# Kernel tuning notes

Hardware: AMD Instinct MI355X
Metric: run time of the kernel (lower is better)

## Reference

```python
import jax, jax.numpy as jnp
import numpy as np

DIM = 768
HEADS = 12
B, H_IMG, W_IMG = 8, 32, 32


def setup_inputs() -> dict:
    key = jax.random.key(0)
    k1, k2, k3 = jax.random.split(key, 3)
    x = jax.random.normal(k1, (B, DIM, H_IMG, W_IMG), dtype=jnp.float32)
    w_qkv = jax.random.normal(k2, (DIM, 3 * DIM), dtype=jnp.float32) * (DIM ** -0.5)
    w_proj = jax.random.normal(k3, (DIM, DIM), dtype=jnp.float32) * (DIM ** -0.5)
    return {"x": x, "w_qkv": w_qkv, "w_proj": w_proj}


def reference(x, w_qkv, w_proj):
    b, c, h, w = x.shape
    n = h * w
    d_head = c // HEADS
    # NOTE: original multiplies energy by sqrt(d_head) (not divides) -- kept faithful.
    scale = d_head ** 0.5

    tokens = x.reshape(b, c, n).transpose(0, 2, 1)          # (b, n, c)
    qkv = tokens @ w_qkv                                     # (b, n, 3c)
    # einops '(d k h)': d outermost, k middle, h innermost
    qkv = qkv.reshape(b, n, d_head, 3, HEADS)
    qkv = jnp.transpose(qkv, (3, 0, 4, 1, 2))                # (3, b, heads, n, d)
    q, k, v = qkv[0], qkv[1], qkv[2]

    energy = jnp.einsum('bhid,bhjd->bhij', q, k) * scale     # (b, heads, n, n)
    attn = jax.nn.softmax(energy, axis=-1)
    ctx = jnp.einsum('bhij,bhjd->bhid', attn, v)             # (b, heads, n, d)
    ctx = jnp.transpose(ctx, (0, 2, 1, 3)).reshape(b, n, c)  # (b, n, c) = (h d) concat
    out = ctx @ w_proj                                       # (b, n, c)
    return jnp.transpose(out.reshape(b, h, w, c), (0, 3, 1, 2))  # (b, c, h, w)
```

## Files before the change

### kernel.cpp

```cpp
#include <hip/hip_runtime.h>

#define NB    8
#define CDIM  768
#define NTOK  1024
#define NHEAD 12
#define DHEAD 64
#define C3    2304

typedef unsigned short u16;
typedef short  s8v __attribute__((ext_vector_type(8)));
typedef float  f4v __attribute__((ext_vector_type(4)));

#define MFMA16(a, b, c) __builtin_amdgcn_mfma_f32_16x16x32_bf16((a), (b), (c), 0, 0, 0)

static __device__ __forceinline__ u16 f2bf(float f) {
    unsigned u = __float_as_uint(f);
    u += 0x7fffu + ((u >> 16) & 1u);
    return (u16)(u >> 16);
}
static __device__ __forceinline__ float bf2f(u16 b) {
    return __uint_as_float(((unsigned)b) << 16);
}
static __device__ __forceinline__ unsigned packsplit(float x) {
    u16 h = f2bf(x);
    u16 l = f2bf(x - bf2f(h));
    return (unsigned)h | ((unsigned)l << 16);
}
static __device__ __forceinline__ void unpack8(uint4 a, uint4 b, s8v& h, s8v& l) {
    h = (s8v){(short)a.x, (short)a.y, (short)a.z, (short)a.w,
              (short)b.x, (short)b.y, (short)b.z, (short)b.w};
    l = (s8v){(short)(a.x >> 16), (short)(a.y >> 16), (short)(a.z >> 16), (short)(a.w >> 16),
              (short)(b.x >> 16), (short)(b.y >> 16), (short)(b.z >> 16), (short)(b.w >> 16)};
}
static __device__ __forceinline__ int sw32i(int row, int k) {
    int g = (k >> 3) & 3;
    int gs = g ^ ((row >> 1) & 3);
    return (k & ~31) + (gs << 3) + (k & 7);
}
static __device__ __forceinline__ void gload16(const u16* gsrc, u16* ldst) {
    __builtin_amdgcn_global_load_lds(
        (const __attribute__((address_space(1))) void*)gsrc,
        (__attribute__((address_space(3))) void*)ldst, 16, 0, 0);
}

__launch_bounds__(256)
__global__ void split_x(const float* __restrict__ x,
                        u16* __restrict__ xh, u16* __restrict__ xl) {
    __shared__ float Tf[64][65];
    const int t  = threadIdx.x;
    const int p0 = blockIdx.x * 64;
    const int c0 = blockIdx.y * 64;
    const int b  = blockIdx.z;

    #pragma unroll
    for (int i = 0; i < 4; ++i) {
        int cl = (t >> 4) + i * 16;
        int pl = (t & 15) * 4;
        float4 v4 = *(const float4*)&x[((size_t)(b * CDIM) + c0 + cl) * NTOK + p0 + pl];
        Tf[cl][pl + 0] = v4.x; Tf[cl][pl + 1] = v4.y;
        Tf[cl][pl + 2] = v4.z; Tf[cl][pl + 3] = v4.w;
    }
    __syncthreads();
    #pragma unroll
    for (int i = 0; i < 4; ++i) {
        int pr = (t >> 4) + i * 16;
        int c4 = (t & 15) * 4;
        u16 hs[4], ls[4];
        #pragma unroll
        for (int j = 0; j < 4; ++j) {
            float val = Tf[c4 + j][pr];
            hs[j] = f2bf(val);
            ls[j] = f2bf(val - bf2f(hs[j]));
        }
        size_t m = (size_t)(b * NTOK) + p0 + pr;
        int ksw = sw32i(p0 + pr, c0 + c4);
        *(ushort4*)&xh[m * CDIM + ksw] = make_ushort4(hs[0], hs[1], hs[2], hs[3]);
        *(ushort4*)&xl[m * CDIM + ksw] = make_ushort4(ls[0], ls[1], ls[2], ls[3]);
    }
}

__launch_bounds__(256)
__global__ void split_w(const float* __restrict__ w,
                        u16* __restrict__ wh, u16* __restrict__ wl) {
    __shared__ float Wf[16][148];
    const int t  = threadIdx.x;
    const int d0 = blockIdx.x * 4;
    const int c0 = blockIdx.y * 16;

    #pragma unroll
    for (int i = 0; i < 9; ++i) {
        int idx = t + i * 256;
        int cl = idx / 144;
        int nl = idx - cl * 144;
        Wf[cl][nl] = w[(size_t)(c0 + cl) * C3 + d0 * 36 + nl];
    }
    __syncthreads();
    #pragma unroll
    for (int i = 0; i < 9; ++i) {
        int idx = t + i * 256;
        int r  = idx >> 4;
        int cc = idx & 15;
        int dd = r / 36;
        int th = r - dd * 36;
        float val = Wf[cc][dd * 36 + th];
        u16 hb = f2bf(val);
        int np = th * 64 + d0 + dd;
        size_t o = (size_t)np * CDIM + sw32i(np, c0 + cc);
        wh[o] = hb;
        wl[o] = f2bf(val - bf2f(hb));
    }
}

__launch_bounds__(256)
__global__ void split_wp(const float* __restrict__ w,
                         u16* __restrict__ wph, u16* __restrict__ wpl) {
    __shared__ float Tf[64][65];
    const int t  = threadIdx.x;
    const int n0 = blockIdx.x * 64;
    const int k0 = blockIdx.y * 64;

    #pragma unroll
    for (int i = 0; i < 4; ++i) {
        int kl = (t >> 4) + i * 16;
        int nl = (t & 15) * 4;
        float4 v4 = *(const float4*)&w[(size_t)(k0 + kl) * CDIM + n0 + nl];
        Tf[kl][nl + 0] = v4.x; Tf[kl][nl + 1] = v4.y;
        Tf[kl][nl + 2] = v4.z; Tf[kl][nl + 3] = v4.w;
    }
    __syncthreads();
    #pragma unroll
    for (int i = 0; i < 4; ++i) {
        int nr = (t >> 4) + i * 16;
        int k4 = (t & 15) * 4;
        u16 hs[4], ls[4];
        #pragma unroll
        for (int j = 0; j < 4; ++j) {
            float val = Tf[k4 + j][nr];
            hs[j] = f2bf(val);
            ls[j] = f2bf(val - bf2f(hs[j]));
        }
        int n = n0 + nr;
        int ksw = sw32i(n, k0 + k4);
        *(ushort4*)&wph[(size_t)n * CDIM + ksw] = make_ushort4(hs[0], hs[1], hs[2], hs[3]);
        *(ushort4*)&wpl[(size_t)n * CDIM + ksw] = make_ushort4(ls[0], ls[1], ls[2], ls[3]);
    }
}

__launch_bounds__(256)
__global__ void qkv_mfma(const u16* __restrict__ xh, const u16* __restrict__ xl,
                         const u16* __restrict__ wh, const u16* __restrict__ wl,
                         unsigned* __restrict__ Qp,
                         u16* __restrict__ Khg, u16* __restrict__ Klg,
                         u16* __restrict__ Vhg, u16* __restrict__ Vlg) {
    __shared__ u16 Ah[128][32];
    __shared__ u16 Al[128][32];
    __shared__ u16 Bh[128][32];
    __shared__ u16 Bl[128][32];

    const int tid = threadIdx.x;
    const int l   = tid & 63;
    const int w   = tid >> 6;
    const int lm  = l & 15;
    const int lg  = l >> 4;
    const int wr  = w >> 1;
    const int wc  = w & 1;
    const int m0  = blockIdx.x * 128;
    const int n0  = blockIdx.y * 128;
    const int b   = m0 >> 10;
    const int p0  = m0 & 1023;

    const size_t xbase = ((size_t)(b * NTOK) + p0) * CDIM;
    const int lrow = l >> 2;
    const int kq   = (l & 3) * 8;
    const int asw  = (lg ^ ((lm >> 1) & 3)) * 8;

    f4v acc[4][4];
    #pragma unroll
    for (int i = 0; i < 4; ++i)
        #pragma unroll
        for (int j = 0; j < 4; ++j)
            acc[i][j] = (f4v){0.f, 0.f, 0.f, 0.f};

    for (int k0 = 0; k0 < CDIM; k0 += 32) {
        #pragma unroll
        for (int i = 0; i < 2; ++i) {
            int ch = w * 2 + i;
            int m  = ch * 16 + lrow;
            int lo = ch * 512;
            gload16(xh + xbase + (size_t)m * CDIM + k0 + kq, &Ah[0][0] + lo);
            gload16(xl + xbase + (size_t)m * CDIM + k0 + kq, &Al[0][0] + lo);
            gload16(wh + (size_t)(n0 + m) * CDIM + k0 + kq,  &Bh[0][0] + lo);
            gload16(wl + (size_t)(n0 + m) * CDIM + k0 + kq,  &Bl[0][0] + lo);
        }
        __syncthreads();

        s8v ah[4], al[4], bh[4], bl[4];
        #pragma unroll
        for (int mi = 0; mi < 4; ++mi) {
            int row = wr * 64 + mi * 16 + lm;
            ah[mi] = *(const s8v*)&Ah[row][asw];
            al[mi] = *(const s8v*)&Al[row][asw];
        }
        #pragma unroll
        for (int ni = 0; ni < 4; ++ni) {
            int row = wc * 64 + ni * 16 + lm;
            bh[ni] = *(const s8v*)&Bh[row][asw];
            bl[ni] = *(const s8v*)&Bl[row][asw];
        }
        #pragma unroll
        for (int mi = 0; mi < 4; ++mi)
            #pragma unroll
            for (int ni = 0; ni < 4; ++ni) {
                acc[mi][ni] = MFMA16(ah[mi], bh[ni], acc[mi][ni]);
                acc[mi][ni] = MFMA16(ah[mi], bl[ni], acc[mi][ni]);
                acc[mi][ni] = MFMA16(al[mi], bh[ni], acc[mi][ni]);
            }
        __syncthreads();
    }

    const int th = (n0 >> 6) + wc;
    const int t3 = th / 12;
    const int h  = th - t3 * 12;
    const size_t bhb = (size_t)(b * NHEAD + h) * NTOK;

    if (t3 == 0) {
        unsigned* dst = Qp + bhb * DHEAD;
        #pragma unroll
        for (int mi = 0; mi < 4; ++mi)
            #pragma unroll
            for (int r = 0; r < 4; ++r) {
                int p = p0 + wr * 64 + mi * 16 + lg * 4 + r;
                #pragma unroll
                for (int ni = 0; ni < 4; ++ni)
                    dst[(size_t)p * DHEAD + ni * 16 + lm] = packsplit(acc[mi][ni][r] * 8.0f);
            }
    } else if (t3 == 1) {
        u16* dh = Khg + bhb * DHEAD;
        u16* dl = Klg + bhb * DHEAD;
        #pragma unroll
        for (int mi = 0; mi < 4; ++mi)
            #pragma unroll
            for (int r = 0; r < 4; ++r) {
                int p = p0 + wr * 64 + mi * 16 + lg * 4 + r;
                #pragma unroll
                for (int ni = 0; ni < 4; ++ni) {
                    int d = ni * 16 + lm;
                    int dsw = (((d >> 3) ^ (p & 7)) << 3) | (d & 7);
                    float val = acc[mi][ni][r];
                    u16 hb = f2bf(val);
                    dh[(size_t)p * DHEAD + dsw] = hb;
                    dl[(size_t)p * DHEAD + dsw] = f2bf(val - bf2f(hb));
                }
            }
    } else {
        u16* dh = Vhg + bhb * DHEAD;
        u16* dl = Vlg + bhb * DHEAD;
        #pragma unroll
        for (int mi = 0; mi < 4; ++mi)
            #pragma unroll
            for (int r = 0; r < 4; ++r) {
                int p = p0 + wr * 64 + mi * 16 + lg * 4 + r;
                #pragma unroll
                for (int ni = 0; ni < 4; ++ni) {
                    int d = ni * 16 + lm;
                    float val = acc[mi][ni][r];
                    u16 hb = f2bf(val);
                    dh[(size_t)p * DHEAD + d] = hb;
                    dl[(size_t)p * DHEAD + d] = f2bf(val - bf2f(hb));
                }
            }
    }
}

__launch_bounds__(256)
__global__ void vt_split(const u16* __restrict__ Vh, const u16* __restrict__ Vl,
                         u16* __restrict__ Vth, u16* __restrict__ Vtl) {
    __shared__ u16 Th[64][72];
    __shared__ u16 Tl[64][72];
    const int t  = threadIdx.x;
    const int pt = blockIdx.x;
    const int bh = blockIdx.y;

    #pragma unroll
    for (int i = 0; i < 4; ++i) {
        int idx = t + i * 256;
        int pr  = idx >> 4;
        int c4  = (idx & 15) * 4;
        size_t src = ((size_t)bh * NTOK + pt * 64 + pr) * DHEAD + c4;
        *(ushort4*)&Th[pr][c4] = *(const ushort4*)&Vh[src];
        *(ushort4*)&Tl[pr][c4] = *(const ushort4*)&Vl[src];
    }
    __syncthreads();
    #pragma unroll
    for (int i = 0; i < 4; ++i) {
        int idx   = t + i * 256;
        int plane = idx >> 9;
        int rem   = idx & 511;
        int d     = rem >> 3;
        int gp    = rem & 7;
        int gs    = gp ^ (d & 7);
        u16 tmp[8];
        #pragma unroll
        for (int j = 0; j < 8; ++j)
            tmp[j] = plane ? Tl[gs * 8 + j][d] : Th[gs * 8 + j][d];
        u16* outp = plane ? Vtl : Vth;
        size_t dst = ((size_t)bh * DHEAD + d) * NTOK + pt * 64 + gp * 8;
        *(ushort4*)&outp[dst]     = make_ushort4(tmp[0], tmp[1], tmp[2], tmp[3]);
        *(ushort4*)&outp[dst + 4] = make_ushort4(tmp[4], tmp[5], tmp[6], tmp[7]);
    }
}

__launch_bounds__(256)
__global__ void attn_mfma(const unsigned* __restrict__ Qp,
                          const u16* __restrict__ Khg, const u16* __restrict__ Klg,
                          const u16* __restrict__ Vth, const u16* __restrict__ Vtl,
                          u16* __restrict__ ctxh, u16* __restrict__ ctxl) {
    __shared__ u16 Kh[64][64];
    __shared__ u16 Kl[64][64];
    __shared__ u16 Vh[64][64];
    __shared__ u16 Vl[64][64];
    __shared__ u16 Ph[128][64];

    const int tid = threadIdx.x;
    const int l  = tid & 63;
    const int w  = tid >> 6;
    const int lm = l & 15;
    const int lg = l >> 4;
    const int bh = blockIdx.y;
    const int p0 = blockIdx.x * 128;

    const unsigned* Qb = Qp + (size_t)bh * NTOK * DHEAD;
    const u16* Kb_h = Khg + (size_t)bh * NTOK * DHEAD;
    const u16* Kb_l = Klg + (size_t)bh * NTOK * DHEAD;
    const u16* Vb_h = Vth + (size_t)bh * DHEAD * NTOK;
    const u16* Vb_l = Vtl + (size_t)bh * DHEAD * NTOK;

    s8v qh[2][2], ql[2][2];
    #pragma unroll
    for (int t = 0; t < 2; ++t)
        #pragma unroll
        for (int kk = 0; kk < 2; ++kk) {
            const unsigned* src = Qb + (size_t)(p0 + w * 32 + t * 16 + lm) * DHEAD + kk * 32 + lg * 8;
            uint4 a0 = *(const uint4*)src;
            uint4 a1 = *(const uint4*)(src + 4);
            unpack8(a0, a1, qh[t][kk], ql[t][kk]);
        }

    f4v o[2][4];
    float mrun[2][4], lrun[2][4];
    #pragma unroll
    for (int t = 0; t < 2; ++t)
        #pragma unroll
        for (int c = 0; c < 4; ++c)
            o[t][c] = (f4v){0.f, 0.f, 0.f, 0.f};
    #pragma unroll
    for (int t = 0; t < 2; ++t)
        #pragma unroll
        for (int i = 0; i < 4; ++i) { mrun[t][i] = -3.0e38f; lrun[t][i] = 0.f; }

    const int fsw = (l & 7) * 8;
    const int r8  = l >> 3;

    for (int kt = 0; kt < 16; ++kt) {
        __syncthreads();
        #pragma unroll
        for (int i = 0; i < 2; ++i) {
            int ch = w * 2 + i;
            int lo = ch * 512;
            size_t krow = (size_t)(kt * 64 + ch * 8 + r8) * DHEAD + fsw;
            gload16(Kb_h + krow, &Kh[0][0] + lo);
            gload16(Kb_l + krow, &Kl[0][0] + lo);
            size_t vrow = (size_t)(ch * 8 + r8) * NTOK + kt * 64 + fsw;
            gload16(Vb_h + vrow, &Vh[0][0] + lo);
            gload16(Vb_l + vrow, &Vl[0][0] + lo);
        }
        __syncthreads();

        f4v sa[2][4];
        #pragma unroll
        for (int t = 0; t < 2; ++t)
            #pragma unroll
            for (int c = 0; c < 4; ++c)
                sa[t][c] = (f4v){0.f, 0.f, 0.f, 0.f};

        #pragma unroll
        for (int kk = 0; kk < 2; ++kk)
            #pragma unroll
            for (int c = 0; c < 4; ++c) {
                int row = c * 16 + lm;
                int off = (((kk * 4 + lg) ^ (lm & 7))) * 8;
                s8v kh = *(const s8v*)&Kh[row][off];
                s8v kl = *(const s8v*)&Kl[row][off];
                #pragma unroll
                for (int t = 0; t < 2; ++t) {
                    sa[t][c] = MFMA16(qh[t][kk], kh, sa[t][c]);
                    sa[t][c] = MFMA16(qh[t][kk], kl, sa[t][c]);
                    sa[t][c] = MFMA16(ql[t][kk], kh, sa[t][c]);
                }
            }

        #pragma unroll
        for (int t = 0; t < 2; ++t) {
            float f_[4];
            #pragma unroll
            for (int i = 0; i < 4; ++i) {
                float mt = fmaxf(fmaxf(sa[t][0][i], sa[t][1][i]),
                                 fmaxf(sa[t][2][i], sa[t][3][i]));
                #pragma unroll
                for (int off = 1; off < 16; off <<= 1)
                    mt = fmaxf(mt, __shfl_xor(mt, off, 16));
                float mn = fmaxf(mrun[t][i], mt);
                f_[i] = __expf(mrun[t][i] - mn);
                mrun[t][i] = mn;
            }
            #pragma unroll
            for (int i = 0; i < 4; ++i) {
                int rp = w * 32 + t * 16 + lg * 4 + i;
                float rs = 0.f;
                #pragma unroll
                for (int c = 0; c < 4; ++c) {
                    float pv = __expf(sa[t][c][i] - mrun[t][i]);
                    rs += pv;
                    int colg = c * 2 + (lm >> 3);
                    Ph[rp][((colg ^ (rp & 7)) << 3) + (lm & 7)] = f2bf(pv);
                }
                #pragma unroll
                for (int off = 1; off < 16; off <<= 1)
                    rs += __shfl_xor(rs, off, 16);
                lrun[t][i] = lrun[t][i] * f_[i] + rs;
                #pragma unroll
                for (int c = 0; c < 4; ++c)
                    o[t][c][i] *= f_[i];
            }
        }

        s8v pf[2][2];
        #pragma unroll
        for (int t = 0; t < 2; ++t)
            #pragma unroll
            for (int kk = 0; kk < 2; ++kk) {
                int row = w * 32 + t * 16 + lm;
                pf[t][kk] = *(const s8v*)&Ph[row][(((kk * 4 + lg) ^ (lm & 7))) * 8];
            }
        #pragma unroll
        for (int c = 0; c < 4; ++c)
            #pragma unroll
            for (int kk = 0; kk < 2; ++kk) {
                int row = c * 16 + lm;
                int off = (((kk * 4 + lg) ^ (lm & 7))) * 8;
                s8v vh = *(const s8v*)&Vh[row][off];
                s8v vl = *(const s8v*)&Vl[row][off];
                #pragma unroll
                for (int t = 0; t < 2; ++t) {
                    o[t][c] = MFMA16(pf[t][kk], vh, o[t][c]);
                    o[t][c] = MFMA16(pf[t][kk], vl, o[t][c]);
                }
            }
    }

    const int b  = bh / NHEAD;
    const int hh = bh - b * NHEAD;
    #pragma unroll
    for (int t = 0; t < 2; ++t)
        #pragma unroll
        for (int i = 0; i < 4; ++i) {
            float inv = 1.f / lrun[t][i];
            int p = p0 + w * 32 + t * 16 + lg * 4 + i;
            size_t m = (size_t)(b * NTOK) + p;
            #pragma unroll
            for (int c = 0; c < 4; ++c) {
                int col = hh * DHEAD + c * 16 + lm;
                int csw = sw32i(p, col);
                float val = o[t][c][i] * inv;
                u16 hb = f2bf(val);
                ctxh[m * CDIM + csw] = hb;
                ctxl[m * CDIM + csw] = f2bf(val - bf2f(hb));
            }
        }
}

__launch_bounds__(256)
__global__ void proj_mfma(const u16* __restrict__ wph, const u16* __restrict__ wpl,
                          const u16* __restrict__ cth, const u16* __restrict__ ctl,
                          float* __restrict__ out) {
    __shared__ u16 Awh[64][32];
    __shared__ u16 Awl[64][32];
    __shared__ u16 Bch[128][32];
    __shared__ u16 Bcl[128][32];

    const int tid = threadIdx.x;
    const int l   = tid & 63;
    const int w   = tid >> 6;
    const int lm  = l & 15;
    const int lg  = l >> 4;
    const int wr  = w >> 1;
    const int wc  = w & 1;
    const int c0  = blockIdx.x * 64;
    const int m0  = blockIdx.y * 128;
    const int b   = m0 >> 10;
    const int pl0 = m0 & 1023;

    const int lrow = l >> 2;
    const int kq   = (l & 3) * 8;
    const int asw  = (lg ^ ((lm >> 1) & 3)) * 8;

    f4v acc[2][4];
    #pragma unroll
    for (int i = 0; i < 2; ++i)
        #pragma unroll
        for (int j = 0; j < 4; ++j)
            acc[i][j] = (f4v){0.f, 0.f, 0.f, 0.f};

    for (int k0 = 0; k0 < CDIM; k0 += 32) {
        {
            int row = w * 16 + lrow;
            gload16(wph + (size_t)(c0 + row) * CDIM + k0 + kq, &Awh[0][0] + w * 512);
            gload16(wpl + (size_t)(c0 + row) * CDIM + k0 + kq, &Awl[0][0] + w * 512);
        }
        #pragma unroll
        for (int i = 0; i < 2; ++i) {
            int ch = w * 2 + i;
            int row = ch * 16 + lrow;
            gload16(cth + (size_t)(m0 + row) * CDIM + k0 + kq, &Bch[0][0] + ch * 512);
            gload16(ctl + (size_t)(m0 + row) * CDIM + k0 + kq, &Bcl[0][0] + ch * 512);
        }
        __syncthreads();

        s8v ah[2], al[2], bh[4], bl[4];
        #pragma unroll
        for (int mi = 0; mi < 2; ++mi) {
            int row = wr * 32 + mi * 16 + lm;
            ah[mi] = *(const s8v*)&Awh[row][asw];
            al[mi] = *(const s8v*)&Awl[row][asw];
        }
        #pragma unroll
        for (int ni = 0; ni < 4; ++ni) {
            int row = wc * 64 + ni * 16 + lm;
            bh[ni] = *(const s8v*)&Bch[row][asw];
            bl[ni] = *(const s8v*)&Bcl[row][asw];
        }
        #pragma unroll
        for (int mi = 0; mi < 2; ++mi)
            #pragma unroll
            for (int ni = 0; ni < 4; ++ni) {
                acc[mi][ni] = MFMA16(ah[mi], bh[ni], acc[mi][ni]);
                acc[mi][ni] = MFMA16(ah[mi], bl[ni], acc[mi][ni]);
                acc[mi][ni] = MFMA16(al[mi], bh[ni], acc[mi][ni]);
            }
        __syncthreads();
    }

    #pragma unroll
    for (int mi = 0; mi < 2; ++mi)
        #pragma unroll
        for (int r = 0; r < 4; ++r) {
            int cpr = c0 + wr * 32 + mi * 16 + lg * 4 + r;
            #pragma unroll
            for (int ni = 0; ni < 4; ++ni) {
                int p = pl0 + wc * 64 + ni * 16 + lm;
                out[((size_t)b * CDIM + cpr) * NTOK + p] = acc[mi][ni][r];
            }
        }
}

extern "C" void kernel_launch(void* const* d_in, const int* in_sizes, int n_in,
                              void* d_out, int out_size, void* d_ws, size_t ws_size,
                              hipStream_t stream) {
    (void)in_sizes; (void)n_in; (void)out_size; (void)ws_size;
    const float* x      = (const float*)d_in[0];
    const float* w_qkv  = (const float*)d_in[1];
    const float* w_proj = (const float*)d_in[2];
    float* out = (float*)d_out;

    const size_t NE = (size_t)NB * NHEAD * NTOK * DHEAD;
    char* w8 = (char*)d_ws;
    unsigned* Qp = (unsigned*)w8;
    u16* Khg = (u16*)(w8 + 4 * NE);
    u16* Klg = Khg + NE;
    u16* Vhg = (u16*)(w8 + 8 * NE);
    u16* Vlg = Vhg + NE;
    u16* xh  = (u16*)(w8 + 12 * NE);
    u16* xl  = xh + NE;
    u16* wh  = (u16*)(w8 + 16 * NE);
    u16* wl  = wh + (size_t)C3 * CDIM;
    u16* Vth  = xh;   u16* Vtl  = xl;
    u16* ctxh = Vhg;  u16* ctxl = Vlg;
    u16* wph  = wh;   u16* wpl  = wh + (size_t)CDIM * CDIM;

    split_x <<<dim3(16, 12, 8), 256, 0, stream>>>(x, xh, xl);
    split_w <<<dim3(16, 48),    256, 0, stream>>>(w_qkv, wh, wl);
    qkv_mfma<<<dim3(64, 18),    256, 0, stream>>>(xh, xl, wh, wl, Qp, Khg, Klg, Vhg, Vlg);
    split_wp<<<dim3(12, 12),    256, 0, stream>>>(w_proj, wph, wpl);
    vt_split<<<dim3(16, 96),    256, 0, stream>>>(Vhg, Vlg, Vth, Vtl);
    attn_mfma<<<dim3(8, 96),    256, 0, stream>>>(Qp, Khg, Klg, Vth, Vtl, ctxh, ctxl);
    proj_mfma<<<dim3(12, 64),   256, 0, stream>>>(wph, wpl, ctxh, ctxl, out);
}
```

Measured before the change: 367.7 us.

## Load K/V directly from global in attention, remap blocks per XCD, use exp2

The attention kernel drops its LDS staging of K and V tiles and the two per-tile barriers, reading MFMA operands straight from global/L2 with unswizzled layouts. Block indices are remapped so that each XCD handles contiguous heads, which should improve L2 reuse of K/V. Q is prescaled by log2(e) so softmax can use exp2f. s_setprio is placed around the MFMA loops in all three GEMM kernels. The costs are uncached, uncoalesced-per-wave global reads of K/V on every tile and more exposed memory latency.

```diff
diff --git a/kernel.cpp b/kernel.cpp
--- a/kernel.cpp
+++ b/kernel.cpp
@@ -12,6 +12,7 @@
 typedef float  f4v __attribute__((ext_vector_type(4)));
 
 #define MFMA16(a, b, c) __builtin_amdgcn_mfma_f32_16x16x32_bf16((a), (b), (c), 0, 0, 0)
+#define LOG2E 1.4426950408889634f
 
 static __device__ __forceinline__ u16 f2bf(float f) {
     unsigned u = __float_as_uint(f);
@@ -207,6 +208,7 @@
             bh[ni] = *(const s8v*)&Bh[row][asw];
             bl[ni] = *(const s8v*)&Bl[row][asw];
         }
+        __builtin_amdgcn_s_setprio(1);
         #pragma unroll
         for (int mi = 0; mi < 4; ++mi)
             #pragma unroll
@@ -215,6 +217,7 @@
                 acc[mi][ni] = MFMA16(ah[mi], bl[ni], acc[mi][ni]);
                 acc[mi][ni] = MFMA16(al[mi], bh[ni], acc[mi][ni]);
             }
+        __builtin_amdgcn_s_setprio(0);
         __syncthreads();
     }
 
@@ -232,29 +235,12 @@
                 int p = p0 + wr * 64 + mi * 16 + lg * 4 + r;
                 #pragma unroll
                 for (int ni = 0; ni < 4; ++ni)
-                    dst[(size_t)p * DHEAD + ni * 16 + lm] = packsplit(acc[mi][ni][r] * 8.0f);
+                    dst[(size_t)p * DHEAD + ni * 16 + lm] =
+                        packsplit(acc[mi][ni][r] * (8.0f * LOG2E));
             }
     } else if (t3 == 1) {
         u16* dh = Khg + bhb * DHEAD;
         u16* dl = Klg + bhb * DHEAD;
-        #pragma unroll
-        for (int mi = 0; mi < 4; ++mi)
-            #pragma unroll
-            for (int r = 0; r < 4; ++r) {
-                int p = p0 + wr * 64 + mi * 16 + lg * 4 + r;
-                #pragma unroll
-                for (int ni = 0; ni < 4; ++ni) {
-                    int d = ni * 16 + lm;
-                    int dsw = (((d >> 3) ^ (p & 7)) << 3) | (d & 7);
-                    float val = acc[mi][ni][r];
-                    u16 hb = f2bf(val);
-                    dh[(size_t)p * DHEAD + dsw] = hb;
-                    dl[(size_t)p * DHEAD + dsw] = f2bf(val - bf2f(hb));
-                }
-            }
-    } else {
-        u16* dh = Vhg + bhb * DHEAD;
-        u16* dl = Vlg + bhb * DHEAD;
         #pragma unroll
         for (int mi = 0; mi < 4; ++mi)
             #pragma unroll
@@ -269,6 +255,23 @@
                     dl[(size_t)p * DHEAD + d] = f2bf(val - bf2f(hb));
                 }
             }
+    } else {
+        u16* dh = Vhg + bhb * DHEAD;
+        u16* dl = Vlg + bhb * DHEAD;
+        #pragma unroll
+        for (int mi = 0; mi < 4; ++mi)
+            #pragma unroll
+            for (int r = 0; r < 4; ++r) {
+                int p = p0 + wr * 64 + mi * 16 + lg * 4 + r;
+                #pragma unroll
+                for (int ni = 0; ni < 4; ++ni) {
+                    int d = ni * 16 + lm;
+                    float val = acc[mi][ni][r];
+                    u16 hb = f2bf(val);
+                    dh[(size_t)p * DHEAD + d] = hb;
+                    dl[(size_t)p * DHEAD + d] = f2bf(val - bf2f(hb));
+                }
+            }
     }
 }
 
@@ -298,11 +301,10 @@
         int rem   = idx & 511;
         int d     = rem >> 3;
         int gp    = rem & 7;
-        int gs    = gp ^ (d & 7);
         u16 tmp[8];
         #pragma unroll
         for (int j = 0; j < 8; ++j)
-            tmp[j] = plane ? Tl[gs * 8 + j][d] : Th[gs * 8 + j][d];
+            tmp[j] = plane ? Tl[gp * 8 + j][d] : Th[gp * 8 + j][d];
         u16* outp = plane ? Vtl : Vth;
         size_t dst = ((size_t)bh * DHEAD + d) * NTOK + pt * 64 + gp * 8;
         *(ushort4*)&outp[dst]     = make_ushort4(tmp[0], tmp[1], tmp[2], tmp[3]);
@@ -315,10 +317,6 @@
                           const u16* __restrict__ Khg, const u16* __restrict__ Klg,
                           const u16* __restrict__ Vth, const u16* __restrict__ Vtl,
                           u16* __restrict__ ctxh, u16* __restrict__ ctxl) {
-    __shared__ u16 Kh[64][64];
-    __shared__ u16 Kl[64][64];
-    __shared__ u16 Vh[64][64];
-    __shared__ u16 Vl[64][64];
     __shared__ u16 Ph[128][64];
 
     const int tid = threadIdx.x;
@@ -326,8 +324,12 @@
     const int w  = tid >> 6;
     const int lm = l & 15;
     const int lg = l >> 4;
-    const int bh = blockIdx.y;
-    const int p0 = blockIdx.x * 128;
+
+    const int bid = blockIdx.x;
+    const int xcd = bid & 7;
+    const int k_  = bid >> 3;
+    const int bh  = xcd * 12 + (k_ >> 3);
+    const int p0  = (k_ & 7) * 128;
 
     const unsigned* Qb = Qp + (size_t)bh * NTOK * DHEAD;
     const u16* Kb_h = Khg + (size_t)bh * NTOK * DHEAD;
@@ -358,23 +360,13 @@
         #pragma unroll
         for (int i = 0; i < 4; ++i) { mrun[t][i] = -3.0e38f; lrun[t][i] = 0.f; }
 
-    const int fsw = (l & 7) * 8;
-    const int r8  = l >> 3;
+    const u16* Krow_h = Kb_h + ((size_t)lm << 6) + lg * 8;
+    const u16* Krow_l = Kb_l + ((size_t)lm << 6) + lg * 8;
+    const u16* Vrow_h = Vb_h + ((size_t)lm << 10) + lg * 8;
+    const u16* Vrow_l = Vb_l + ((size_t)lm << 10) + lg * 8;
 
     for (int kt = 0; kt < 16; ++kt) {
-        __syncthreads();
-        #pragma unroll
-        for (int i = 0; i < 2; ++i) {
-            int ch = w * 2 + i;
-            int lo = ch * 512;
-            size_t krow = (size_t)(kt * 64 + ch * 8 + r8) * DHEAD + fsw;
-            gload16(Kb_h + krow, &Kh[0][0] + lo);
-            gload16(Kb_l + krow, &Kl[0][0] + lo);
-            size_t vrow = (size_t)(ch * 8 + r8) * NTOK + kt * 64 + fsw;
-            gload16(Vb_h + vrow, &Vh[0][0] + lo);
-            gload16(Vb_l + vrow, &Vl[0][0] + lo);
-        }
-        __syncthreads();
+        const int kv0 = kt * 64;
 
         f4v sa[2][4];
         #pragma unroll
@@ -387,16 +379,17 @@
         for (int kk = 0; kk < 2; ++kk)
             #pragma unroll
             for (int c = 0; c < 4; ++c) {
-                int row = c * 16 + lm;
-                int off = (((kk * 4 + lg) ^ (lm & 7))) * 8;
-                s8v kh = *(const s8v*)&Kh[row][off];
-                s8v kl = *(const s8v*)&Kl[row][off];
+                size_t off = (size_t)(kv0 + c * 16) * DHEAD + kk * 32;
+                s8v kh = *(const s8v*)(Krow_h + off);
+                s8v kl = *(const s8v*)(Krow_l + off);
+                __builtin_amdgcn_s_setprio(1);
                 #pragma unroll
                 for (int t = 0; t < 2; ++t) {
                     sa[t][c] = MFMA16(qh[t][kk], kh, sa[t][c]);
                     sa[t][c] = MFMA16(qh[t][kk], kl, sa[t][c]);
                     sa[t][c] = MFMA16(ql[t][kk], kh, sa[t][c]);
                 }
+                __builtin_amdgcn_s_setprio(0);
             }
 
         #pragma unroll
@@ -410,7 +403,7 @@
                 for (int off = 1; off < 16; off <<= 1)
                     mt = fmaxf(mt, __shfl_xor(mt, off, 16));
                 float mn = fmaxf(mrun[t][i], mt);
-                f_[i] = __expf(mrun[t][i] - mn);
+                f_[i] = exp2f(mrun[t][i] - mn);
                 mrun[t][i] = mn;
             }
             #pragma unroll
@@ -419,7 +412,7 @@
                 float rs = 0.f;
                 #pragma unroll
                 for (int c = 0; c < 4; ++c) {
-                    float pv = __expf(sa[t][c][i] - mrun[t][i]);
+                    float pv = exp2f(sa[t][c][i] - mrun[t][i]);
                     rs += pv;
                     int colg = c * 2 + (lm >> 3);
                     Ph[rp][((colg ^ (rp & 7)) << 3) + (lm & 7)] = f2bf(pv);
@@ -446,15 +439,16 @@
         for (int c = 0; c < 4; ++c)
             #pragma unroll
             for (int kk = 0; kk < 2; ++kk) {
-                int row = c * 16 + lm;
-                int off = (((kk * 4 + lg) ^ (lm & 7))) * 8;
-                s8v vh = *(const s8v*)&Vh[row][off];
-                s8v vl = *(const s8v*)&Vl[row][off];
+                size_t off = (size_t)(c * 16) * NTOK + kv0 + kk * 32;
+                s8v vh = *(const s8v*)(Vrow_h + off);
+                s8v vl = *(const s8v*)(Vrow_l + off);
+                __builtin_amdgcn_s_setprio(1);
                 #pragma unroll
                 for (int t = 0; t < 2; ++t) {
                     o[t][c] = MFMA16(pf[t][kk], vh, o[t][c]);
                     o[t][c] = MFMA16(pf[t][kk], vl, o[t][c]);
                 }
+                __builtin_amdgcn_s_setprio(0);
             }
     }
 
@@ -539,6 +533,7 @@
             bh[ni] = *(const s8v*)&Bch[row][asw];
             bl[ni] = *(const s8v*)&Bcl[row][asw];
         }
+        __builtin_amdgcn_s_setprio(1);
         #pragma unroll
         for (int mi = 0; mi < 2; ++mi)
             #pragma unroll
@@ -547,6 +542,7 @@
                 acc[mi][ni] = MFMA16(ah[mi], bl[ni], acc[mi][ni]);
                 acc[mi][ni] = MFMA16(al[mi], bh[ni], acc[mi][ni]);
             }
+        __builtin_amdgcn_s_setprio(0);
         __syncthreads();
     }
 
@@ -592,6 +588,6 @@
     qkv_mfma<<<dim3(64, 18),    256, 0, stream>>>(xh, xl, wh, wl, Qp, Khg, Klg, Vhg, Vlg);
     split_wp<<<dim3(12, 12),    256, 0, stream>>>(w_proj, wph, wpl);
     vt_split<<<dim3(16, 96),    256, 0, stream>>>(Vhg, Vlg, Vth, Vtl);
-    attn_mfma<<<dim3(8, 96),    256, 0, stream>>>(Qp, Khg, Klg, Vth, Vtl, ctxh, ctxl);
+    attn_mfma<<<dim3(768),      256, 0, stream>>>(Qp, Khg, Klg, Vth, Vtl, ctxh, ctxl);
     proj_mfma<<<dim3(12, 64),   256, 0, stream>>>(wph, wpl, ctxh, ctxl, out);
 }
```

Result: slower. 472.6 us (+28.5%).
